# Kernel tuning notes

Measured on AMD Instinct MI355X. Metric: run time of the kernel, lower is better.

Reference implementation:

```python
import jax, jax.numpy as jnp
import numpy as np

STEP = 0.1  # step_size from init
H = 2048    # ceil(dim/2)


def setup_inputs() -> dict:
    key = jax.random.key(0)
    k1, k2, k3 = jax.random.split(key, 3)
    B, h = 16384, H
    x = jax.random.normal(k1, (B, 2 * h), dtype=jnp.float32)
    # Xavier-uniform-like scale for [2h, h] linear weights
    scale = (6.0 / (h + 2 * h)) ** 0.5
    W0 = jax.random.normal(k2, (2 * h, h), dtype=jnp.float32) * scale
    W1 = jax.random.normal(k3, (2 * h, h), dtype=jnp.float32) * scale
    b0 = jnp.zeros((2 * h,), dtype=jnp.float32)
    b1 = jnp.zeros((2 * h,), dtype=jnp.float32)
    return {"x": x, "W0": W0, "b0": b0, "W1": W1, "b1": b1}


def reference(x, W0, b0, W1, b1):
    h = W0.shape[1]
    u_old = x[:, :h]          # [B, h]
    v_old = x[:, h:]          # [B, h]
    # stage 1: Linear(u) -> tanh -> W1^T matmul -> scaled residual add
    v_mid = jnp.tanh(u_old @ W1.T + b1)   # [B, 2h]
    v_sig = v_mid @ W1                     # [B, h]  (tied-weight transpose matmul)
    v_new = v_old + STEP * v_sig
    # stage 2: Linear(v_new) -> tanh -> W0^T matmul -> scaled residual sub
    u_mid = jnp.tanh(v_new @ W0.T + b0)   # [B, 2h]
    u_sig = u_mid @ W0                     # [B, h]
    u_new = u_old - STEP * u_sig
    return jnp.concatenate((u_new, v_new), axis=1)
```

## Files before the change

kernel.cpp:

```cpp
#include <hip/hip_runtime.h>
#include <hip/hip_bf16.h>
#include <stdint.h>


typedef __attribute__((ext_vector_type(8))) short short8;
typedef __attribute__((ext_vector_type(4))) float f32x4;

#define DEVINL __device__ __forceinline__

DEVINL ushort f2b(float f) {
  union { float f; uint32_t u; } v; v.f = f;
  uint32_t u = v.u;
  return (ushort)((u + 0x7fffu + ((u >> 16) & 1u)) >> 16);
}

DEVINL float fast_tanh(float x) {
  x = fminf(10.0f, fmaxf(-10.0f, x));
  float e = __expf(2.0f * x);
  return (e - 1.0f) * __builtin_amdgcn_rcpf(e + 1.0f);
}

DEVINL void gload16(const ushort* g, ushort* l) {
  __builtin_amdgcn_global_load_lds(
      (const __attribute__((address_space(1))) void*)g,
      (__attribute__((address_space(3))) void*)l, 16, 0, 0);
}

template<int MH, int NH>
DEVINL void mfma_quad(f32x4 (&acc)[8][4], const short8 (&a)[4][2],
                      const short8 (&b)[2][2]) {
#pragma unroll
  for (int ks = 0; ks < 2; ++ks)
#pragma unroll
    for (int mi = 0; mi < 4; ++mi)
#pragma unroll
      for (int ni = 0; ni < 2; ++ni)
        acc[MH * 4 + mi][NH * 2 + ni] = __builtin_amdgcn_mfma_f32_16x16x32_bf16(
            a[mi][ks], b[ni][ks], acc[MH * 4 + mi][NH * 2 + ni], 0, 0, 0);
}

template<int MODE, int SUPER>
DEVINL void gemm_body(const ushort* __restrict__ A, const ushort* __restrict__ Bt,
                      const float* __restrict__ bias, ushort* __restrict__ Tout,
                      const float* __restrict__ xres, float* __restrict__ outres,
                      ushort* __restrict__ vbout, float step, int M, int N, int K)
{
  __shared__ __align__(16) ushort ldsU[32768];

  const int tid  = threadIdx.x;
  const int wave = tid >> 6, lane = tid & 63;
  const int wr = wave >> 2, wc = wave & 3;
  const int lr = lane & 15, hi = lane >> 4;

  const int GX = gridDim.x;
  const int nwg = GX * gridDim.y;
  const int lin = blockIdx.y * GX + blockIdx.x;
  const int swz = (lin & 7) * (nwg >> 3) + (lin >> 3);
  int bx, by;
  if (SUPER) {
    const int st = swz >> 4, wi = swz & 15;
    const int nsx = GX >> 2;
    bx = (st % nsx) * 4 + (wi & 3);
    by = (st / nsx) * 4 + (wi >> 2);
  } else {
    by = swz / GX; bx = swz - by * GX;
  }
  const int m0 = by * 256, n0 = bx * 256;

  const int kb_st = ((tid & 7) * 16) ^ (((tid >> 3) & 7) << 4);
  int offA[2][2], offB[2][2];
#pragma unroll
  for (int j = 0; j < 2; ++j) {
    const int rp = j * 64 + (tid >> 3);
#pragma unroll
    for (int h = 0; h < 2; ++h) {
      offA[h][j] = (m0 + (rp >> 6) * 128 + h * 64 + (rp & 63)) * K + (kb_st >> 1);
      offB[h][j] = (n0 + (rp >> 5) * 64 + h * 32 + (rp & 31)) * K + (kb_st >> 1);
    }
  }

#define STAGE_A(half, t) do {                                                  \
    gload16(A + (size_t)offA[half][0] + (size_t)(t) * 64,                      \
            ldsU + (half) * 8192 + tid * 8);                                   \
    gload16(A + (size_t)offA[half][1] + (size_t)(t) * 64,                      \
            ldsU + (half) * 8192 + 4096 + tid * 8);                            \
  } while (0)
#define STAGE_B(half, t) do {                                                  \
    gload16(Bt + (size_t)offB[half][0] + (size_t)(t) * 64,                     \
            ldsU + 16384 + (half) * 8192 + tid * 8);                           \
    gload16(Bt + (size_t)offB[half][1] + (size_t)(t) * 64,                     \
            ldsU + 16384 + (half) * 8192 + 4096 + tid * 8);                    \
  } while (0)

  const int xm = (lane & 7) << 4;
  const int kbr0 = (hi * 16) ^ xm;
  const int kbr1 = (64 + hi * 16) ^ xm;
  const int eA0 = (wr * 64 + lr) * 64 + (kbr0 >> 1);
  const int eA1 = (wr * 64 + lr) * 64 + (kbr1 >> 1);
  const int eB0 = (wc * 32 + lr) * 64 + (kbr0 >> 1);
  const int eB1 = (wc * 32 + lr) * 64 + (kbr1 >> 1);

#define LDSE(idx) (*(const short8*)&ldsU[idx])
#define READ_A8(dst, half) do {                                                \
    dst[0][0] = LDSE((half)*8192 +    0 + eA0);                                \
    dst[0][1] = LDSE((half)*8192 +    0 + eA1);                                \
    dst[1][0] = LDSE((half)*8192 + 1024 + eA0);                                \
    dst[1][1] = LDSE((half)*8192 + 1024 + eA1);                                \
    dst[2][0] = LDSE((half)*8192 + 2048 + eA0);                                \
    dst[2][1] = LDSE((half)*8192 + 2048 + eA1);                                \
    dst[3][0] = LDSE((half)*8192 + 3072 + eA0);                                \
    dst[3][1] = LDSE((half)*8192 + 3072 + eA1);                                \
  } while (0)
#define READ_B4(dst, half) do {                                                \
    dst[0][0] = LDSE(16384 + (half)*8192 +    0 + eB0);                        \
    dst[0][1] = LDSE(16384 + (half)*8192 +    0 + eB1);                        \
    dst[1][0] = LDSE(16384 + (half)*8192 + 1024 + eB0);                        \
    dst[1][1] = LDSE(16384 + (half)*8192 + 1024 + eB1);                        \
  } while (0)

  f32x4 acc[8][4] = {};
  short8 a0[4][2], a1[4][2], b0[2][2], b1[2][2];

#define VMW(n) asm volatile("s_waitcnt vmcnt(" #n ")" ::: "memory")
#define LGK0 asm volatile("s_waitcnt lgkmcnt(0)" ::: "memory")
#define SCB __builtin_amdgcn_sched_barrier(0)
#define BAR __builtin_amdgcn_s_barrier()

  const int NT = K >> 6;

  STAGE_A(0, 0); STAGE_A(1, 0); STAGE_B(0, 0);
  STAGE_B(1, 0);
#pragma unroll 1
  for (int t = 0; t < NT - 1; ++t) {
    VMW(2); BAR; SCB;
    READ_A8(a0, 0); READ_B4(b0, 0); READ_A8(a1, 1);
    LGK0; SCB;
    BAR; SCB;
    STAGE_A(0, t + 1); STAGE_A(1, t + 1); STAGE_B(0, t + 1);
    mfma_quad<0, 0>(acc, a0, b0); mfma_quad<1, 0>(acc, a1, b0);
    VMW(6); BAR; SCB;
    READ_B4(b1, 1);
    LGK0; SCB;
    BAR; SCB;
    STAGE_B(1, t + 1);
    mfma_quad<0, 1>(acc, a0, b1); mfma_quad<1, 1>(acc, a1, b1);
  }
  VMW(2); BAR; SCB;
  READ_A8(a0, 0); READ_B4(b0, 0); READ_A8(a1, 1);
  LGK0; SCB;
  mfma_quad<0, 0>(acc, a0, b0); mfma_quad<1, 0>(acc, a1, b0);
  VMW(0); BAR; SCB;
  READ_B4(b1, 1);
  LGK0; SCB;
  mfma_quad<0, 1>(acc, a0, b1); mfma_quad<1, 1>(acc, a1, b1);

  const int mrow0 = m0 + wr * 128 + hi * 4;
  const int ncol0 = n0 + wc * 64 + lr;
  if (MODE == 0) {
    float bv[4];
#pragma unroll
    for (int ni = 0; ni < 4; ++ni) bv[ni] = bias[ncol0 + ni * 16];
#pragma unroll
    for (int mi = 0; mi < 8; ++mi) {
#pragma unroll
      for (int r = 0; r < 4; ++r) {
        const int row = mrow0 + mi * 16 + r;
#pragma unroll
        for (int ni = 0; ni < 4; ++ni)
          Tout[(size_t)row * N + ncol0 + ni * 16] =
              f2b(fast_tanh(acc[mi][ni][r] + bv[ni]));
      }
    }
  } else {
#pragma unroll
    for (int mi = 0; mi < 8; ++mi) {
#pragma unroll
      for (int r = 0; r < 4; ++r) {
        const int row = mrow0 + mi * 16 + r;
#pragma unroll
        for (int ni = 0; ni < 4; ++ni) {
          const size_t oi = (size_t)row * 4096 + ncol0 + ni * 16;
          const float v = fmaf(step, acc[mi][ni][r], xres[oi]);
          outres[oi] = v;
          if (MODE == 1) vbout[(size_t)row * N + ncol0 + ni * 16] = f2b(v);
        }
      }
    }
  }
#undef STAGE_A
#undef STAGE_B
#undef LDSE
#undef READ_A8
#undef READ_B4
#undef VMW
#undef LGK0
#undef SCB
#undef BAR
}

__global__ __launch_bounds__(512, 2)
void gemm_t1(const ushort* A, const ushort* Bt, const float* bias,
             ushort* Tout, int M, int N, int K) {
  gemm_body<0, 1>(A, Bt, bias, Tout, nullptr, nullptr, nullptr, 0.f, M, N, K);
}
__global__ __launch_bounds__(512, 2)
void gemm_vnew(const ushort* A, const ushort* Bt, const float* xres,
               float* outres, ushort* vbout, float step, int M, int N, int K) {
  gemm_body<1, 0>(A, Bt, nullptr, nullptr, xres, outres, vbout, step, M, N, K);
}
__global__ __launch_bounds__(512, 2)
void gemm_t2(const ushort* A, const ushort* Bt, const float* bias,
             ushort* Tout, int M, int N, int K) {
  gemm_body<0, 0>(A, Bt, bias, Tout, nullptr, nullptr, nullptr, 0.f, M, N, K);
}
__global__ __launch_bounds__(512, 2)
void gemm_unew(const ushort* A, const ushort* Bt, const float* xres,
               float* outres, float step, int M, int N, int K) {
  gemm_body<2, 0>(A, Bt, nullptr, nullptr, xres, outres, nullptr, step, M, N, K);
}

__global__ void cast_strided_half(const float* __restrict__ x,
                                  ushort* __restrict__ dst)
{
  const int i = blockIdx.x * blockDim.x + threadIdx.x;
  const int row = i >> 8;
  const int c8  = (i & 255) * 8;
  const float4 v0 = *(const float4*)&x[(size_t)row * 4096 + c8];
  const float4 v1 = *(const float4*)&x[(size_t)row * 4096 + c8 + 4];
  short8 o;
  o[0] = (short)f2b(v0.x); o[1] = (short)f2b(v0.y);
  o[2] = (short)f2b(v0.z); o[3] = (short)f2b(v0.w);
  o[4] = (short)f2b(v1.x); o[5] = (short)f2b(v1.y);
  o[6] = (short)f2b(v1.z); o[7] = (short)f2b(v1.w);
  *(short8*)&dst[(size_t)row * 2048 + c8] = o;
}

__global__ void pack_both(const float* __restrict__ W0, const float* __restrict__ W1,
                          ushort* __restrict__ W0b, ushort* __restrict__ W0t,
                          ushort* __restrict__ W1b, ushort* __restrict__ W1t)
{
  const float* W = blockIdx.z ? W1 : W0;
  ushort* Wb = blockIdx.z ? W1b : W0b;
  ushort* Wt = blockIdx.z ? W1t : W0t;
  __shared__ float tile[32][33];
  const int bx = blockIdx.x * 32;
  const int by = blockIdx.y * 32;
  const int tx = threadIdx.x, ty = threadIdx.y;
#pragma unroll
  for (int j = ty; j < 32; j += 8) {
    const float v = W[(size_t)(by + j) * 2048 + bx + tx];
    tile[j][tx] = v;
    Wb[(size_t)(by + j) * 2048 + bx + tx] = f2b(v);
  }
  __syncthreads();
#pragma unroll
  for (int j = ty; j < 32; j += 8) {
    Wt[(size_t)(bx + j) * 4096 + by + tx] = f2b(tile[tx][j]);
  }
}

extern "C" void kernel_launch(void* const* d_in, const int* in_sizes, int n_in,
                              void* d_out, int out_size, void* d_ws, size_t ws_size,
                              hipStream_t stream)
{
  const float* x  = (const float*)d_in[0];
  const float* W0 = (const float*)d_in[1];
  const float* b0 = (const float*)d_in[2];
  const float* W1 = (const float*)d_in[3];
  const float* b1 = (const float*)d_in[4];
  float* out = (float*)d_out;

  const int Mrows = 16384, H2 = 4096, Hh = 2048;

  uint8_t* ws = (uint8_t*)d_ws;
  ushort* T   = (ushort*)ws;
  ushort* Ab  = (ushort*)(ws + (size_t)134217728);
  ushort* W0b = (ushort*)(ws + (size_t)134217728 + 67108864);
  ushort* W0t = W0b + 8388608;
  ushort* W1b = W0t + 8388608;
  ushort* W1t = W1b + 8388608;

  cast_strided_half<<<16384, 256, 0, stream>>>(x, Ab);
  dim3 pw_grid(64, 128, 2), pw_blk(32, 8);
  pack_both<<<pw_grid, pw_blk, 0, stream>>>(W0, W1, W0b, W0t, W1b, W1t);

  dim3 blk(512);
  dim3 g1(H2 / 256, Mrows / 256);
  dim3 g2(Hh / 256, Mrows / 256);

  gemm_t1<<<g1, blk, 0, stream>>>(Ab, W1b, b1, T, Mrows, H2, Hh);
  gemm_vnew<<<g2, blk, 0, stream>>>(T, W1t, x + Hh, out + Hh, Ab, 0.1f,
                                    Mrows, Hh, H2);
  gemm_t2<<<g1, blk, 0, stream>>>(Ab, W0b, b0, T, Mrows, H2, Hh);
  gemm_unew<<<g2, blk, 0, stream>>>(T, W0t, x, out, -0.1f, Mrows, Hh, H2);
}
```

Before: 1.085 ms.

## Double-buffer the second B half in LDS to drop a barrier per k-tile

Adds a template mode that gives the second half of the B tile two LDS slots, so the next tile's B1 load can be issued early and one block barrier per k-step goes away. The k-loop is unrolled by two with alternating buffer parity. This mode is enabled for the t2 GEMM only. The 4x4 supertile block swizzle, which previously only t1 used, now applies to every GEMM. The cost is more LDS per block (80KB vs 64KB), which could limit occupancy at two blocks per CU.

```diff
diff --git a/kernel.cpp b/kernel.cpp
--- a/kernel.cpp
+++ b/kernel.cpp
@@ -39,13 +39,14 @@
             a[mi][ks], b[ni][ks], acc[MH * 4 + mi][NH * 2 + ni], 0, 0, 0);
 }
 
-template<int MODE, int SUPER>
+template<int MODE, int BDB>
 DEVINL void gemm_body(const ushort* __restrict__ A, const ushort* __restrict__ Bt,
                       const float* __restrict__ bias, ushort* __restrict__ Tout,
                       const float* __restrict__ xres, float* __restrict__ outres,
                       ushort* __restrict__ vbout, float step, int M, int N, int K)
 {
-  __shared__ __align__(16) ushort ldsU[32768];
+  constexpr int LDS_N = BDB ? 40960 : 32768;
+  __shared__ __align__(16) ushort ldsU[LDS_N];
 
   const int tid  = threadIdx.x;
   const int wave = tid >> 6, lane = tid & 63;
@@ -56,15 +57,10 @@
   const int nwg = GX * gridDim.y;
   const int lin = blockIdx.y * GX + blockIdx.x;
   const int swz = (lin & 7) * (nwg >> 3) + (lin >> 3);
-  int bx, by;
-  if (SUPER) {
-    const int st = swz >> 4, wi = swz & 15;
-    const int nsx = GX >> 2;
-    bx = (st % nsx) * 4 + (wi & 3);
-    by = (st / nsx) * 4 + (wi >> 2);
-  } else {
-    by = swz / GX; bx = swz - by * GX;
-  }
+  const int st = swz >> 4, wi = swz & 15;
+  const int nsx = GX >> 2;
+  const int bx = (st % nsx) * 4 + (wi & 3);
+  const int by = (st / nsx) * 4 + (wi >> 2);
   const int m0 = by * 256, n0 = bx * 256;
 
   const int kb_st = ((tid & 7) * 16) ^ (((tid >> 3) & 7) << 4);
@@ -85,11 +81,17 @@
     gload16(A + (size_t)offA[half][1] + (size_t)(t) * 64,                      \
             ldsU + (half) * 8192 + 4096 + tid * 8);                            \
   } while (0)
-#define STAGE_B(half, t) do {                                                  \
-    gload16(Bt + (size_t)offB[half][0] + (size_t)(t) * 64,                     \
-            ldsU + 16384 + (half) * 8192 + tid * 8);                           \
-    gload16(Bt + (size_t)offB[half][1] + (size_t)(t) * 64,                     \
-            ldsU + 16384 + (half) * 8192 + 4096 + tid * 8);                    \
+#define STAGE_B0(t) do {                                                       \
+    gload16(Bt + (size_t)offB[0][0] + (size_t)(t) * 64,                        \
+            ldsU + 16384 + tid * 8);                                           \
+    gload16(Bt + (size_t)offB[0][1] + (size_t)(t) * 64,                        \
+            ldsU + 16384 + 4096 + tid * 8);                                    \
+  } while (0)
+#define STAGE_B1(par, t) do {                                                  \
+    gload16(Bt + (size_t)offB[1][0] + (size_t)(t) * 64,                        \
+            ldsU + 24576 + (par) * 8192 + tid * 8);                            \
+    gload16(Bt + (size_t)offB[1][1] + (size_t)(t) * 64,                        \
+            ldsU + 24576 + (par) * 8192 + 4096 + tid * 8);                     \
   } while (0)
 
   const int xm = (lane & 7) << 4;
@@ -111,11 +113,17 @@
     dst[3][0] = LDSE((half)*8192 + 3072 + eA0);                                \
     dst[3][1] = LDSE((half)*8192 + 3072 + eA1);                                \
   } while (0)
-#define READ_B4(dst, half) do {                                                \
-    dst[0][0] = LDSE(16384 + (half)*8192 +    0 + eB0);                        \
-    dst[0][1] = LDSE(16384 + (half)*8192 +    0 + eB1);                        \
-    dst[1][0] = LDSE(16384 + (half)*8192 + 1024 + eB0);                        \
-    dst[1][1] = LDSE(16384 + (half)*8192 + 1024 + eB1);                        \
+#define READ_B0(dst) do {                                                      \
+    dst[0][0] = LDSE(16384 +    0 + eB0);                                      \
+    dst[0][1] = LDSE(16384 +    0 + eB1);                                      \
+    dst[1][0] = LDSE(16384 + 1024 + eB0);                                      \
+    dst[1][1] = LDSE(16384 + 1024 + eB1);                                      \
+  } while (0)
+#define READ_B1(dst, par) do {                                                 \
+    dst[0][0] = LDSE(24576 + (par)*8192 +    0 + eB0);                         \
+    dst[0][1] = LDSE(24576 + (par)*8192 +    0 + eB1);                         \
+    dst[1][0] = LDSE(24576 + (par)*8192 + 1024 + eB0);                         \
+    dst[1][1] = LDSE(24576 + (par)*8192 + 1024 + eB1);                         \
   } while (0)
 
   f32x4 acc[8][4] = {};
@@ -127,32 +135,63 @@
 #define BAR __builtin_amdgcn_s_barrier()
 
   const int NT = K >> 6;
-
-  STAGE_A(0, 0); STAGE_A(1, 0); STAGE_B(0, 0);
-  STAGE_B(1, 0);
+  const int NI = NT >> 1;
+
+  if constexpr (BDB == 0) {
+    STAGE_A(0, 0); STAGE_A(1, 0); STAGE_B0(0);
+    STAGE_B1(0, 0);
 #pragma unroll 1
-  for (int t = 0; t < NT - 1; ++t) {
+    for (int t = 0; t < NT - 1; ++t) {
+      VMW(2); BAR; SCB;
+      READ_A8(a0, 0); READ_B0(b0); READ_A8(a1, 1);
+      LGK0; SCB;
+      BAR; SCB;
+      STAGE_A(0, t + 1); STAGE_A(1, t + 1); STAGE_B0(t + 1);
+      mfma_quad<0, 0>(acc, a0, b0); mfma_quad<1, 0>(acc, a1, b0);
+      VMW(6); BAR; SCB;
+      READ_B1(b1, 0);
+      LGK0; SCB;
+      BAR; SCB;
+      STAGE_B1(0, t + 1);
+      mfma_quad<0, 1>(acc, a0, b1); mfma_quad<1, 1>(acc, a1, b1);
+    }
     VMW(2); BAR; SCB;
-    READ_A8(a0, 0); READ_B4(b0, 0); READ_A8(a1, 1);
+    READ_A8(a0, 0); READ_B0(b0); READ_A8(a1, 1);
     LGK0; SCB;
-    BAR; SCB;
-    STAGE_A(0, t + 1); STAGE_A(1, t + 1); STAGE_B(0, t + 1);
     mfma_quad<0, 0>(acc, a0, b0); mfma_quad<1, 0>(acc, a1, b0);
-    VMW(6); BAR; SCB;
-    READ_B4(b1, 1);
+    VMW(0); BAR; SCB;
+    READ_B1(b1, 0);
     LGK0; SCB;
-    BAR; SCB;
-    STAGE_B(1, t + 1);
     mfma_quad<0, 1>(acc, a0, b1); mfma_quad<1, 1>(acc, a1, b1);
-  }
-  VMW(2); BAR; SCB;
-  READ_A8(a0, 0); READ_B4(b0, 0); READ_A8(a1, 1);
-  LGK0; SCB;
-  mfma_quad<0, 0>(acc, a0, b0); mfma_quad<1, 0>(acc, a1, b0);
-  VMW(0); BAR; SCB;
-  READ_B4(b1, 1);
-  LGK0; SCB;
-  mfma_quad<0, 1>(acc, a0, b1); mfma_quad<1, 1>(acc, a1, b1);
+  } else {
+#define V3B_TILE(par, STG, VN1, VN2)                                           \
+    VMW(VN1); BAR; SCB;                                                        \
+    READ_A8(a0, 0); READ_B0(b0); READ_A8(a1, 1);                               \
+    LGK0; SCB;                                                                 \
+    BAR; SCB;                                                                  \
+    STG;                                                                       \
+    mfma_quad<0, 0>(acc, a0, b0); mfma_quad<1, 0>(acc, a1, b0);                \
+    VMW(VN2); BAR; SCB;                                                        \
+    READ_B1(b1, par);                                                          \
+    LGK0; SCB;                                                                 \
+    mfma_quad<0, 1>(acc, a0, b1); mfma_quad<1, 1>(acc, a1, b1);
+#define STG8(par_next, t) do {                                                 \
+    STAGE_A(0, t); STAGE_A(1, t); STAGE_B0(t);                                 \
+    STAGE_B1(par_next, t);                                                     \
+  } while (0)
+
+    STG8(0, 0);
+#pragma unroll 1
+    for (int i = 0; i < NI - 1; ++i) {
+      const int t = 2 * i;
+      V3B_TILE(0, STG8(1, t + 1), 2, 8)
+      V3B_TILE(1, STG8(0, t + 2), 2, 8)
+    }
+    V3B_TILE(0, STG8(1, NT - 1), 2, 8)
+    V3B_TILE(1, , 2, 0)
+#undef V3B_TILE
+#undef STG8
+  }
 
   const int mrow0 = m0 + wr * 128 + hi * 4;
   const int ncol0 = n0 + wc * 64 + lr;
@@ -188,10 +227,12 @@
     }
   }
 #undef STAGE_A
-#undef STAGE_B
+#undef STAGE_B0
+#undef STAGE_B1
 #undef LDSE
 #undef READ_A8
-#undef READ_B4
+#undef READ_B0
+#undef READ_B1
 #undef VMW
 #undef LGK0
 #undef SCB
@@ -201,7 +242,7 @@
 __global__ __launch_bounds__(512, 2)
 void gemm_t1(const ushort* A, const ushort* Bt, const float* bias,
              ushort* Tout, int M, int N, int K) {
-  gemm_body<0, 1>(A, Bt, bias, Tout, nullptr, nullptr, nullptr, 0.f, M, N, K);
+  gemm_body<0, 0>(A, Bt, bias, Tout, nullptr, nullptr, nullptr, 0.f, M, N, K);
 }
 __global__ __launch_bounds__(512, 2)
 void gemm_vnew(const ushort* A, const ushort* Bt, const float* xres,
@@ -211,7 +252,7 @@
 __global__ __launch_bounds__(512, 2)
 void gemm_t2(const ushort* A, const ushort* Bt, const float* bias,
              ushort* Tout, int M, int N, int K) {
-  gemm_body<0, 0>(A, Bt, bias, Tout, nullptr, nullptr, nullptr, 0.f, M, N, K);
+  gemm_body<0, 1>(A, Bt, bias, Tout, nullptr, nullptr, nullptr, 0.f, M, N, K);
 }
 __global__ __launch_bounds__(512, 2)
 void gemm_unew(const ushort* A, const ushort* Bt, const float* xres,
```

Result: slower. 1.169 ms (+7.7%).
